# Optimization experiments

Hardware: AMD Instinct MI355X
Metric: run time of the kernel (lower is better)

The kernel has to match this reference:

```python
import jax, jax.numpy as jnp
import numpy as np

B, S, F = 4, 4096, 1024
H, DK, R = 16, 64, 32  # n_head, d_k, low_rank; n_attn = H*DK = 1024


def _l2norm(x, eps=1e-12):
    # torch.nn.functional.normalize(p=2, dim=-1)
    n = jnp.sqrt(jnp.sum(x * x, axis=-1, keepdims=True))
    return x / jnp.maximum(n, eps)


def setup_inputs() -> dict:
    key = jax.random.key(0)
    ks = jax.random.split(key, 16)
    s = 0.02
    inp = {
        "query": jax.random.normal(ks[0], (B, S, F), jnp.float32),
        "key": jax.random.normal(ks[1], (B, S, F), jnp.float32),
        "value": jax.random.normal(ks[2], (B, S, F), jnp.float32),
        "p_layer": 1,
        # linear_q / linear_k (linear_v unused in p_layer branch but kept for fidelity)
        "Wq": jax.random.normal(ks[3], (H * DK, F), jnp.float32) * s,
        "bq": jnp.zeros((H * DK,), jnp.float32),
        "Wk": jax.random.normal(ks[4], (H * DK, F), jnp.float32) * s,
        "bk": jnp.zeros((H * DK,), jnp.float32),
        "Wv": jax.random.normal(ks[5], (H * DK, F), jnp.float32) * s,
        "bv": jnp.zeros((H * DK,), jnp.float32),
        # low-rank projections (orthogonal-init stand-ins)
        "We": jax.random.normal(ks[6], (H, DK, R), jnp.float32) * s,
        "Wr": jax.random.normal(ks[7], (H, DK, R), jnp.float32) * s,
        "Lam": jax.random.uniform(ks[8], (H, R), jnp.float32),
        # concate_weight: Linear(2R -> DK)
        "Wc": jax.random.normal(ks[9], (DK, 2 * R), jnp.float32) * s,
        "bc": jnp.zeros((DK,), jnp.float32),
        # linear_out: Linear(H*DK -> F)
        "Wo": jax.random.normal(ks[10], (F, H * DK), jnp.float32) * s,
        "bo": jnp.zeros((F,), jnp.float32),
    }
    return inp


def reference(query, key, value, Wq, bq, Wk, bk, Wv, bv, We, Wr, Lam, Wc, bc, Wo, bo, p_layer):
    n_batch, seq_len, _ = query.shape
    # projections -> (B, H, S, DK)
    q = (query @ Wq.T + bq).reshape(n_batch, seq_len, H, DK).transpose(0, 2, 1, 3)
    k = (key @ Wk.T + bk).reshape(n_batch, seq_len, H, DK).transpose(0, 2, 1, 3)
    if p_layer:  # static Python int
        normal = jnp.arange(1, seq_len + 1, dtype=q.dtype)[None, None, :, None]
        q = jnp.cumsum(q, axis=2) / normal  # causal running average
        k = jnp.cumsum(k, axis=2) / normal
        q = _l2norm(q)
        k = _l2norm(k)
        escore = jnp.einsum('bhnd,hde->bhne', q, We)  # (B,H,S,R)
        rscore = jnp.einsum('bhnd,hde->bhne', k, Wr)
        scores = jnp.concatenate((escore, rscore), axis=-1)  # (B,H,S,2R)
        x = scores @ Wc.T + bc  # (B,H,S,DK)
        x = x.transpose(0, 2, 1, 3).reshape(n_batch, seq_len, H * DK)
    else:
        v = (value @ Wv.T + bv).reshape(n_batch, seq_len, H, DK).transpose(0, 2, 1, 3)
        att = jax.nn.softmax(jnp.einsum('bhqd,bhkd->bhqk', q, k) / jnp.sqrt(jnp.asarray(DK, q.dtype)), axis=-1)
        x = jnp.einsum('bhqk,bhkd->bhqd', att, v).transpose(0, 2, 1, 3).reshape(n_batch, seq_len, H * DK)
    return x @ Wo.T + bo
```

## Files before the change

kernel.cpp:

```cpp
#include <hip/hip_runtime.h>

typedef __bf16 bf16x8 __attribute__((ext_vector_type(8)));
typedef float floatx4 __attribute__((ext_vector_type(4)));

__device__ __forceinline__ unsigned short f2bf(float x) {
  union { float f; unsigned u; } v; v.f = x;
  unsigned u = v.u;
  unsigned r = (u + 0x7FFFu + ((u >> 16) & 1u)) >> 16;
  return (unsigned short)r;
}
__device__ __forceinline__ float bf2f(unsigned short x) {
  union { unsigned u; float f; } v; v.u = ((unsigned)x) << 16;
  return v.f;
}
__device__ __forceinline__ float fast_rcp(float x) {
#if defined(__has_builtin) && __has_builtin(__builtin_amdgcn_rcpf)
  return __builtin_amdgcn_rcpf(x);
#else
  return 1.0f / x;
#endif
}
__device__ __forceinline__ float fast_rsq(float x) {
#if defined(__has_builtin) && __has_builtin(__builtin_amdgcn_rsqf)
  return __builtin_amdgcn_rsqf(x);
#else
  return 1.0f / sqrtf(x);
#endif
}

__device__ __forceinline__ void stage16(const unsigned short* __restrict__ g,
                                        unsigned short* s, int lane) {
#if defined(__has_builtin) && __has_builtin(__builtin_amdgcn_global_load_lds)
  __builtin_amdgcn_global_load_lds((const __attribute__((address_space(1))) void*)g,
                                   (__attribute__((address_space(3))) void*)s,
                                   16, 0, 0);
#else
  *(uint4*)(s + (size_t)lane * 8) = *(const uint4*)g;
#endif
}

__global__ void cvt_bf16(const float* __restrict__ in, unsigned short* __restrict__ out, int n4) {
  int i = blockIdx.x * 256 + threadIdx.x;
  if (i >= n4) return;
  const float4 v = ((const float4*)in)[i];
  ushort4 o;
  o.x = f2bf(v.x); o.y = f2bf(v.y); o.z = f2bf(v.z); o.w = f2bf(v.w);
  ((ushort4*)out)[i] = o;
}

#define LDSE (256 * 64)

#define RD_A(b, mh) {                                                          \
  _Pragma("unroll") for (int ii = 0; ii < 4; ++ii) {                           \
    _Pragma("unroll") for (int s = 0; s < 2; ++s) {                            \
      af[ii][s] = *(const bf16x8*)(rA + (b) * LDSE +                           \
                                   ((mh) * 128 + ii * 16) * 64 +               \
                                   (((s << 2) | quad) ^ key) * 8);             \
    } } }

#define RD_B(b, nh, dst) {                                                     \
  _Pragma("unroll") for (int jj = 0; jj < 2; ++jj) {                           \
    _Pragma("unroll") for (int s = 0; s < 2; ++s) {                            \
      dst[jj][s] = *(const bf16x8*)(rB + (b) * LDSE +                          \
                                    ((nh) * 128 + jj * 16) * 64 +              \
                                    (((s << 2) | quad) ^ key) * 8);            \
    } } }

#define STAGE_A(b, mh, t) {                                                    \
  stage16(gA + (size_t)((mh) * 128) * K + (size_t)(t) * 64,                    \
          sAw + (b) * LDSE + ((mh) * 128) * 64, lane);                         \
  stage16(gA + (size_t)((mh) * 128 + 8) * K + (size_t)(t) * 64,                \
          sAw + (b) * LDSE + ((mh) * 128 + 8) * 64, lane); }

#define STAGE_B(b, nh, t) {                                                    \
  stage16(gB + (size_t)((nh) * 128) * K + (size_t)(t) * 64,                    \
          sBw + (b) * LDSE + ((nh) * 128) * 64, lane);                         \
  stage16(gB + (size_t)((nh) * 128 + 8) * K + (size_t)(t) * 64,                \
          sBw + (b) * LDSE + ((nh) * 128 + 8) * 64, lane); }

#define MFMA_PH(mh, nh, bfx) {                                                 \
  __builtin_amdgcn_s_setprio(1);                                               \
  _Pragma("unroll") for (int s = 0; s < 2; ++s) {                              \
    _Pragma("unroll") for (int ii = 0; ii < 4; ++ii) {                         \
      _Pragma("unroll") for (int jj = 0; jj < 2; ++jj) {                       \
        acc[mh][nh][ii][jj] = __builtin_amdgcn_mfma_f32_16x16x32_bf16(         \
            af[ii][s], bfx[jj][s], acc[mh][nh][ii][jj], 0, 0, 0);              \
      } } }                                                                    \
  __builtin_amdgcn_s_setprio(0); }

#define TILE(b, t, S1, S234, MORE) {                                           \
                                  \
  RD_B(b, 0, bf0); RD_A(b, 0);                                                 \
  if (S1) { STAGE_A((b) ^ 1, 1, (t) + 1); }                                    \
  MFMA_PH(0, 0, bf0);                                                          \
  __builtin_amdgcn_s_barrier();                                                \
                                     \
  RD_B(b, 1, bf1);                                                             \
  if (S234) { STAGE_A(b, 0, (t) + 2); }                                        \
  MFMA_PH(0, 1, bf1);                                                          \
  __builtin_amdgcn_s_barrier();                                                \
                                     \
  RD_A(b, 1);                                                                  \
  if (S234) { STAGE_B(b, 0, (t) + 2); }                                        \
  MFMA_PH(1, 1, bf1);                                                          \
  __builtin_amdgcn_s_barrier();                                                \
                                 \
  if (S234) { STAGE_B(b, 1, (t) + 2); }                                        \
  MFMA_PH(1, 0, bf0);                                                          \
  if (MORE) { asm volatile("s_waitcnt vmcnt(6)" ::: "memory"); }               \
  else      { asm volatile("s_waitcnt vmcnt(0)" ::: "memory"); }               \
  __builtin_amdgcn_s_barrier(); }

template <int OUT_BF16>
__global__ __launch_bounds__(512, 2) void gemm8p(const unsigned short* __restrict__ A,
                                                 const unsigned short* __restrict__ B,
                                                 const float* __restrict__ bias,
                                                 void* __restrict__ Cv,
                                                 int M, int N, int K) {
  __shared__ unsigned short As[2 * 256 * 64];
  __shared__ unsigned short Bs[2 * 256 * 64];
  const int tid = threadIdx.x;
  const int w = tid >> 6;
  const int lane = tid & 63;

  const int NT = N >> 8;
  const int id = blockIdx.x;
  const int x = id & 7;
  const int g = id >> 3;
  const int nt_ = g % NT;
  const int mt = x + 8 * (g / NT);
  const int bm = mt * 256, bn = nt_ * 256;

  const int row16 = lane & 15, quad = lane >> 4, key = lane & 7;
  const int l8 = lane >> 3, lk = lane & 7;
  const int swz = (lk ^ l8) * 8;

  const unsigned short* gA = A + (size_t)(bm + 16 * w + l8) * K + swz;
  const unsigned short* gB = B + (size_t)(bn + 16 * w + l8) * K + swz;
  unsigned short* sAw = As + (16 * w) * 64;
  unsigned short* sBw = Bs + (16 * w) * 64;

  const unsigned short* rA = As + ((w >> 2) * 64 + row16) * 64;
  const unsigned short* rB = Bs + ((w & 3) * 32 + row16) * 64;

  floatx4 acc[2][2][4][2] = {};
  bf16x8 af[4][2], bf0[2][2], bf1[2][2];

  STAGE_A(0, 0, 0); STAGE_B(0, 0, 0); STAGE_B(0, 1, 0); STAGE_A(0, 1, 0);
  STAGE_A(1, 0, 1); STAGE_B(1, 0, 1); STAGE_B(1, 1, 1);
  asm volatile("s_waitcnt vmcnt(6)" ::: "memory");
  __builtin_amdgcn_s_barrier();

  const int npair = K >> 7;
  for (int it = 0; it < npair; ++it) {
    const int t0 = it * 2;
    const bool more = (it + 1 < npair);
    TILE(0, t0, true, more, more);
    TILE(1, t0 + 1, more, more, more);
  }

#pragma unroll
  for (int nh = 0; nh < 2; ++nh)
#pragma unroll
    for (int jj = 0; jj < 2; ++jj) {
      const int gcol = bn + nh * 128 + (w & 3) * 32 + jj * 16 + row16;
      const float bb = bias ? bias[gcol] : 0.0f;
#pragma unroll
      for (int mh = 0; mh < 2; ++mh)
#pragma unroll
        for (int ii = 0; ii < 4; ++ii) {
          const int grow = bm + mh * 128 + (w >> 2) * 64 + ii * 16 + quad * 4;
#pragma unroll
          for (int r = 0; r < 4; ++r) {
            float v = acc[mh][nh][ii][jj][r] + bb;
            if (OUT_BF16)
              ((unsigned short*)Cv)[(size_t)(grow + r) * N + gcol] = f2bf(v);
            else
              ((float*)Cv)[(size_t)(grow + r) * N + gcol] = v;
          }
        }
    }
}

__global__ void scan_partial(const unsigned short* __restrict__ proj, float* __restrict__ partial) {
  const int t = blockIdx.x, chunk = blockIdx.y, b = blockIdx.z;
  const int c4 = threadIdx.x * 4;
  const unsigned short* p =
      proj + ((size_t)t * 4 + b) * 4096 * 1024 + (size_t)chunk * 64 * 1024 + c4;
  float4 s = {0.f, 0.f, 0.f, 0.f};
  for (int i = 0; i < 64; i++) {
    const ushort4 v = *(const ushort4*)(p + (size_t)i * 1024);
    s.x += bf2f(v.x); s.y += bf2f(v.y); s.z += bf2f(v.z); s.w += bf2f(v.w);
  }
  *(float4*)(partial + ((size_t)(t * 4 + b) * 64 + chunk) * 1024 + c4) = s;
}

__global__ void scan_apply(const unsigned short* __restrict__ proj,
                           const float* __restrict__ partial,
                           unsigned short* __restrict__ qkn) {
  const int t = blockIdx.x, chunk = blockIdx.y, b = blockIdx.z;
  const int c4 = threadIdx.x * 4;
  const float* pp = partial + (size_t)(t * 4 + b) * 64 * 1024 + c4;
  float4 run = {0.f, 0.f, 0.f, 0.f};
  for (int j = 0; j < chunk; j++) {
    const float4 v = *(const float4*)(pp + (size_t)j * 1024);
    run.x += v.x; run.y += v.y; run.z += v.z; run.w += v.w;
  }
  const unsigned short* p =
      proj + ((size_t)t * 4 + b) * 4096 * 1024 + (size_t)chunk * 64 * 1024 + c4;
  unsigned short* o = qkn + (size_t)b * 4096 * 2048 + (size_t)chunk * 64 * 2048 + t * 1024 + c4;
  for (int i = 0; i < 64; i++) {
    const ushort4 v = *(const ushort4*)(p + (size_t)i * 1024);
    run.x += bf2f(v.x); run.y += bf2f(v.y); run.z += bf2f(v.z); run.w += bf2f(v.w);
    const int s = chunk * 64 + i;
    const float inv = fast_rcp((float)(s + 1));
    const float a0 = run.x * inv, a1 = run.y * inv, a2 = run.z * inv, a3 = run.w * inv;
    float sq = a0 * a0 + a1 * a1 + a2 * a2 + a3 * a3;
    sq += __shfl_xor(sq, 8);
    sq += __shfl_xor(sq, 4);
    sq += __shfl_xor(sq, 2);
    sq += __shfl_xor(sq, 1);
    const float sc = fast_rsq(fmaxf(sq, 1e-24f));
    ushort4 ov;
    ov.x = f2bf(a0 * sc); ov.y = f2bf(a1 * sc); ov.z = f2bf(a2 * sc); ov.w = f2bf(a3 * sc);
    *(ushort4*)(o + (size_t)i * 2048) = ov;
  }
}

__global__ void make_A(const float* __restrict__ We, const float* __restrict__ Wr,
                       const float* __restrict__ Wc, float* __restrict__ Asm) {
  const int t = blockIdx.x >> 4, h = blockIdx.x & 15;
  const float* W = (t ? Wr : We) + (size_t)h * 64 * 32;
  for (int e = threadIdx.x; e < 4096; e += 256) {
    const int d = e >> 6, dk = e & 63;
    float s = 0.f;
    for (int r = 0; r < 32; r++) s += W[d * 32 + r] * Wc[dk * 64 + t * 32 + r];
    Asm[(size_t)blockIdx.x * 4096 + e] = s;
  }
}

__global__ __launch_bounds__(256) void make_G(const float* __restrict__ Asm,
                                              const float* __restrict__ Wo,
                                              unsigned short* __restrict__ Gt) {
  __shared__ float At[64 * 65];
  __shared__ float WoSh[64 * 64];
  const int th = blockIdx.x, t = th >> 4, h = th & 15;
  const int f0 = blockIdx.y * 64;
  const int tid = threadIdx.x;
  for (int e = tid; e < 4096; e += 256) {
    const int d = e >> 6, dk = e & 63;
    At[dk * 65 + d] = Asm[(size_t)th * 4096 + e];
  }
  for (int e = tid; e < 4096; e += 256) {
    const int fl = e >> 6, dk = e & 63;
    WoSh[e] = Wo[(size_t)(f0 + fl) * 1024 + h * 64 + dk];
  }
  __syncthreads();
  const int d = tid & 63;
  const int fsub = tid >> 6;
#pragma unroll 4
  for (int it = 0; it < 16; ++it) {
    const int fl = it * 4 + fsub;
    float s = 0.f;
#pragma unroll
    for (int dk4 = 0; dk4 < 16; ++dk4) {
      const float4 wv = *(const float4*)&WoSh[fl * 64 + dk4 * 4];
      s += At[(dk4 * 4 + 0) * 65 + d] * wv.x + At[(dk4 * 4 + 1) * 65 + d] * wv.y +
           At[(dk4 * 4 + 2) * 65 + d] * wv.z + At[(dk4 * 4 + 3) * 65 + d] * wv.w;
    }
    Gt[(size_t)(f0 + fl) * 2048 + t * 1024 + h * 64 + d] = f2bf(s);
  }
}

__global__ void make_c0(const float* __restrict__ bc, const float* __restrict__ bo,
                        const float* __restrict__ Wo, float* __restrict__ c0) {
  const int f = blockIdx.x * 4 + (threadIdx.x >> 6);
  const int lane = threadIdx.x & 63;
  const float bcl = bc[lane];
  float s = 0.f;
  for (int j = lane; j < 1024; j += 64) s += bcl * Wo[(size_t)f * 1024 + j];
#pragma unroll
  for (int off = 32; off; off >>= 1) s += __shfl_xor(s, off);
  if (lane == 0) c0[f] = s + bo[f];
}

extern "C" void kernel_launch(void* const* d_in, const int* in_sizes, int n_in,
                              void* d_out, int out_size, void* d_ws, size_t ws_size,
                              hipStream_t stream) {
  const float* query = (const float*)d_in[0];
  const float* key_  = (const float*)d_in[1];
  const float* Wq = (const float*)d_in[4];
  const float* bq = (const float*)d_in[5];
  const float* Wk = (const float*)d_in[6];
  const float* bk = (const float*)d_in[7];
  const float* We = (const float*)d_in[10];
  const float* Wr = (const float*)d_in[11];
  const float* Wc = (const float*)d_in[13];
  const float* bc = (const float*)d_in[14];
  const float* Wo = (const float*)d_in[15];
  const float* bo = (const float*)d_in[16];

  char* ws = (char*)d_ws;
  unsigned short* qkbf = (unsigned short*)ws;
  unsigned short* Wbf  = (unsigned short*)(ws + 67108864);
  unsigned short* Gt   = (unsigned short*)(ws + 71303168);
  float* partial       = (float*)(ws + 71303168);
  float* Asm           = (float*)(ws + 75497472);
  float* c0            = (float*)(ws + 76021760);

  unsigned short* proj = (unsigned short*)d_out;

  cvt_bf16<<<16384, 256, 0, stream>>>(query, qkbf, 4194304);
  cvt_bf16<<<16384, 256, 0, stream>>>(key_, qkbf + 16777216, 4194304);
  cvt_bf16<<<1024, 256, 0, stream>>>(Wq, Wbf, 262144);
  cvt_bf16<<<1024, 256, 0, stream>>>(Wk, Wbf + 1048576, 262144);

  gemm8p<1><<<256, 512, 0, stream>>>(qkbf, Wbf, bq, proj, 16384, 1024, 1024);
  gemm8p<1><<<256, 512, 0, stream>>>(qkbf + 16777216, Wbf + 1048576, bk,
                                     proj + 16777216, 16384, 1024, 1024);

  scan_partial<<<dim3(2, 64, 4), 256, 0, stream>>>(proj, partial);
  scan_apply<<<dim3(2, 64, 4), 256, 0, stream>>>(proj, partial, qkbf);

  make_A<<<32, 256, 0, stream>>>(We, Wr, Wc, Asm);
  make_G<<<dim3(32, 16), 256, 0, stream>>>(Asm, Wo, Gt);
  make_c0<<<256, 256, 0, stream>>>(bc, bo, Wo, c0);

  gemm8p<0><<<256, 512, 0, stream>>>(qkbf, Gt, c0, (float*)d_out, 16384, 1024, 2048);
}
```

Before: 450.4 us.

## Merge Q/K projection GEMMs into one launch and simplify pipeline to one barrier per tile

The separate Q and K projection GEMM launches become a single 512-block launch. Each block picks its weight matrix and bias by its row range, which removes one launch and tail and gives a fuller grid. The GEMM main loop also drops the fine-grained staged prefetch with three intermediate barriers. It now issues the whole next tile's loads at the start of each tile and waits with vmcnt(0) plus one barrier at the end. This cuts barrier overhead but shortens the prefetch distance from two tiles to one, so global loads may be less hidden behind MFMA work.

```diff
diff --git a/kernel.cpp b/kernel.cpp
--- a/kernel.cpp
+++ b/kernel.cpp
@@ -49,6 +49,7 @@
 }
 
 #define LDSE (256 * 64)
+#define BAR() __builtin_amdgcn_s_barrier()
 
 #define RD_A(b, mh) {                                                          \
   _Pragma("unroll") for (int ii = 0; ii < 4; ++ii) {                           \
@@ -88,35 +89,26 @@
       } } }                                                                    \
   __builtin_amdgcn_s_setprio(0); }
 
-#define TILE(b, t, S1, S234, MORE) {                                           \
-                                  \
+#define TILE5(b, t, S, Y) {                                                    \
+  if (S) { STAGE_A((b) ^ 1, 0, (t) + 1); STAGE_B((b) ^ 1, 0, (t) + 1);         \
+           STAGE_B((b) ^ 1, 1, (t) + 1); STAGE_A((b) ^ 1, 1, (t) + 1); }       \
   RD_B(b, 0, bf0); RD_A(b, 0);                                                 \
-  if (S1) { STAGE_A((b) ^ 1, 1, (t) + 1); }                                    \
   MFMA_PH(0, 0, bf0);                                                          \
-  __builtin_amdgcn_s_barrier();                                                \
-                                     \
   RD_B(b, 1, bf1);                                                             \
-  if (S234) { STAGE_A(b, 0, (t) + 2); }                                        \
   MFMA_PH(0, 1, bf1);                                                          \
-  __builtin_amdgcn_s_barrier();                                                \
-                                     \
   RD_A(b, 1);                                                                  \
-  if (S234) { STAGE_B(b, 0, (t) + 2); }                                        \
   MFMA_PH(1, 1, bf1);                                                          \
-  __builtin_amdgcn_s_barrier();                                                \
-                                 \
-  if (S234) { STAGE_B(b, 1, (t) + 2); }                                        \
   MFMA_PH(1, 0, bf0);                                                          \
-  if (MORE) { asm volatile("s_waitcnt vmcnt(6)" ::: "memory"); }               \
-  else      { asm volatile("s_waitcnt vmcnt(0)" ::: "memory"); }               \
-  __builtin_amdgcn_s_barrier(); }
+  if (Y) { asm volatile("s_waitcnt vmcnt(0)" ::: "memory"); BAR(); } }
 
 template <int OUT_BF16>
 __global__ __launch_bounds__(512, 2) void gemm8p(const unsigned short* __restrict__ A,
                                                  const unsigned short* __restrict__ B,
+                                                 const unsigned short* __restrict__ B2,
                                                  const float* __restrict__ bias,
+                                                 const float* __restrict__ bias2,
                                                  void* __restrict__ Cv,
-                                                 int M, int N, int K) {
+                                                 int M, int N, int K, int halfM) {
   __shared__ unsigned short As[2 * 256 * 64];
   __shared__ unsigned short Bs[2 * 256 * 64];
   const int tid = threadIdx.x;
@@ -131,12 +123,15 @@
   const int mt = x + 8 * (g / NT);
   const int bm = mt * 256, bn = nt_ * 256;
 
+  const unsigned short* Bp = (bm >= halfM) ? B2 : B;
+  const float* biasp = (bm >= halfM) ? bias2 : bias;
+
   const int row16 = lane & 15, quad = lane >> 4, key = lane & 7;
   const int l8 = lane >> 3, lk = lane & 7;
   const int swz = (lk ^ l8) * 8;
 
   const unsigned short* gA = A + (size_t)(bm + 16 * w + l8) * K + swz;
-  const unsigned short* gB = B + (size_t)(bn + 16 * w + l8) * K + swz;
+  const unsigned short* gB = Bp + (size_t)(bn + 16 * w + l8) * K + swz;
   unsigned short* sAw = As + (16 * w) * 64;
   unsigned short* sBw = Bs + (16 * w) * 64;
 
@@ -147,24 +142,23 @@
   bf16x8 af[4][2], bf0[2][2], bf1[2][2];
 
   STAGE_A(0, 0, 0); STAGE_B(0, 0, 0); STAGE_B(0, 1, 0); STAGE_A(0, 1, 0);
-  STAGE_A(1, 0, 1); STAGE_B(1, 0, 1); STAGE_B(1, 1, 1);
-  asm volatile("s_waitcnt vmcnt(6)" ::: "memory");
-  __builtin_amdgcn_s_barrier();
+  asm volatile("s_waitcnt vmcnt(0)" ::: "memory");
+  BAR();
 
   const int npair = K >> 7;
-  for (int it = 0; it < npair; ++it) {
-    const int t0 = it * 2;
-    const bool more = (it + 1 < npair);
-    TILE(0, t0, true, more, more);
-    TILE(1, t0 + 1, more, more, more);
-  }
+  for (int it = 0; it < npair - 1; ++it) {
+    TILE5(0, 2 * it, true, true);
+    TILE5(1, 2 * it + 1, true, true);
+  }
+  TILE5(0, 2 * npair - 2, true, true);
+  TILE5(1, 2 * npair - 1, false, false);
 
 #pragma unroll
   for (int nh = 0; nh < 2; ++nh)
 #pragma unroll
     for (int jj = 0; jj < 2; ++jj) {
       const int gcol = bn + nh * 128 + (w & 3) * 32 + jj * 16 + row16;
-      const float bb = bias ? bias[gcol] : 0.0f;
+      const float bb = biasp ? biasp[gcol] : 0.0f;
 #pragma unroll
       for (int mh = 0; mh < 2; ++mh)
 #pragma unroll
@@ -315,9 +309,8 @@
   cvt_bf16<<<1024, 256, 0, stream>>>(Wq, Wbf, 262144);
   cvt_bf16<<<1024, 256, 0, stream>>>(Wk, Wbf + 1048576, 262144);
 
-  gemm8p<1><<<256, 512, 0, stream>>>(qkbf, Wbf, bq, proj, 16384, 1024, 1024);
-  gemm8p<1><<<256, 512, 0, stream>>>(qkbf + 16777216, Wbf + 1048576, bk,
-                                     proj + 16777216, 16384, 1024, 1024);
+  gemm8p<1><<<512, 512, 0, stream>>>(qkbf, Wbf, Wbf + 1048576, bq, bk, proj,
+                                     32768, 1024, 1024, 16384);
 
   scan_partial<<<dim3(2, 64, 4), 256, 0, stream>>>(proj, partial);
   scan_apply<<<dim3(2, 64, 4), 256, 0, stream>>>(proj, partial, qkbf);
@@ -326,5 +319,6 @@
   make_G<<<dim3(32, 16), 256, 0, stream>>>(Asm, Wo, Gt);
   make_c0<<<256, 256, 0, stream>>>(bc, bo, Wo, c0);
 
-  gemm8p<0><<<256, 512, 0, stream>>>(qkbf, Gt, c0, (float*)d_out, 16384, 1024, 2048);
-}
+  gemm8p<0><<<256, 512, 0, stream>>>(qkbf, Gt, Gt, c0, c0, (float*)d_out,
+                                     16384, 1024, 2048, 16384 * 2);
+}
```

Result: no change. 446.9 us (-0.8%).
